# Kernel tuning notes

Measured on AMD Instinct MI355X. Metric: run time of the kernel, lower is better.

The kernel has to match this reference:

```python
import jax, jax.numpy as jnp
import numpy as np

N_NODES = 50000
IN_CH = 256
N_REL = 5
N_EDGES = 800000
LAST_SENSES = 25000
LAST_GLOBALS = 45000


def setup_inputs() -> dict:
    key = jax.random.key(0)
    ks = jax.random.split(key, 12)
    batch_x = jax.random.normal(ks[0], (N_NODES, IN_CH), dtype=jnp.float32)
    batch_edge_index = jax.random.randint(ks[1], (2, N_EDGES), 0, N_NODES)
    batch_edge_type = jax.random.randint(ks[2], (N_EDGES,), 0, N_REL)
    s = 1.0 / np.sqrt(IN_CH)
    comp = jax.random.normal(ks[3], (N_REL, N_REL), dtype=jnp.float32) * (1.0 / np.sqrt(N_REL))
    basis = jax.random.normal(ks[4], (N_REL, IN_CH, IN_CH), dtype=jnp.float32) * s
    root = jax.random.normal(ks[5], (IN_CH, IN_CH), dtype=jnp.float32) * s
    bias = jnp.zeros((IN_CH,), dtype=jnp.float32)
    n_glob = LAST_GLOBALS - LAST_SENSES
    Wg = jax.random.normal(ks[6], (n_glob, IN_CH), dtype=jnp.float32) * s
    bg = jnp.zeros((n_glob,), dtype=jnp.float32)
    Ws = jax.random.normal(ks[7], (LAST_SENSES, IN_CH), dtype=jnp.float32) * s
    bs = jnp.zeros((LAST_SENSES,), dtype=jnp.float32)
    return {
        'batch_x': batch_x,
        'batch_edge_index': batch_edge_index,
        'batch_edge_type': batch_edge_type,
        'comp': comp,
        'basis': basis,
        'root': root,
        'bias': bias,
        'Wg': Wg,
        'bg': bg,
        'Ws': Ws,
        'bs': bs,
    }


def _rgcn_conv(x, edge_index, edge_type, comp, basis, root, bias):
    # Basis decomposition: W_r = sum_b comp[r,b] * basis[b]  -> [R, d, d]
    R = comp.shape[0]
    N = x.shape[0]
    W = jnp.einsum('rb,bdf->rdf', comp, basis)
    # Transform all nodes by every relation weight once ([R,N,F]), then gather
    # per edge instead of doing an [E,d,d] weight gather.
    H = jnp.einsum('nd,rdf->rnf', x, W)
    src, dst = edge_index[0], edge_index[1]
    msgs = H[edge_type, src]                     # [E, F]
    seg = edge_type * N + dst                    # combined (relation, dst) id
    sums = jax.ops.segment_sum(msgs, seg, num_segments=R * N)
    cnt = jax.ops.segment_sum(jnp.ones((msgs.shape[0],), msgs.dtype), seg,
                              num_segments=R * N)
    mean = sums / jnp.maximum(cnt, 1.0)[:, None]  # per-relation mean aggregation
    agg = mean.reshape(R, N, -1).sum(axis=0)
    return agg + x @ root + bias


def reference(batch_x, batch_edge_index, batch_edge_type, comp, basis, root,
              bias, Wg, bg, Ws, bs):
    h = jax.nn.relu(_rgcn_conv(batch_x, batch_edge_index, batch_edge_type,
                               comp, basis, root, bias))
    x1 = h[0]                                    # current node embedding [F]
    logits_global = Wg @ x1 + bg
    logits_sense = Ws @ x1 + bs
    return (jax.nn.log_softmax(logits_global, axis=0),
            jax.nn.log_softmax(logits_sense, axis=0))
```

## Files before the change

kernel.cpp:

```cpp
#include <hip/hip_runtime.h>
#include <math.h>

#define N_NODES 50000
#define IN_CH 256
#define N_REL 5
#define N_EDGES 800000
#define N_GLOB 20000
#define N_SENSE 25000
#define N_OUT 45000
#define MAX_MATCH 256
#define NBLK_LOGITS (N_OUT / 4)
#define NBLK_GLOB (N_GLOB / 4)


__global__ void k_W(const float* __restrict__ comp,
                    const float* __restrict__ basis,
                    float* __restrict__ W,
                    float* __restrict__ sums,
                    int* __restrict__ ip) {
    int t = threadIdx.x, bid = blockIdx.x;
    if (bid == 0 && t < 8) ip[t] = 0;
    if (bid < 5) sums[bid * 256 + t] = 0.f;
    int idx = bid * 256 + t;
    int r = idx >> 16, df = idx & 65535;
    float acc = 0.f;
#pragma unroll
    for (int b = 0; b < N_REL; ++b)
        acc += comp[r * N_REL + b] * basis[b * (IN_CH * IN_CH) + df];
    W[idx] = acc;
}

__device__ __forceinline__ void record_edge(const int* ei, const int* et,
                                            int* ip, int e) {
    int t = et[e];
    int p = atomicAdd(&ip[0], 1);
    if (p < MAX_MATCH) {
        ip[8 + p] = ei[e];
        ip[8 + MAX_MATCH + p] = t;
    }
    atomicAdd(&ip[1 + t], 1);
}

__global__ void k_scan(const int* __restrict__ ei,
                       const int* __restrict__ et,
                       int* __restrict__ ip) {
    int e4 = blockIdx.x * 256 + threadIdx.x;
    if (e4 * 4 >= N_EDGES) return;
    int4 d = ((const int4*)(ei + N_EDGES))[e4];
    int e = e4 * 4;
    if (d.x == 0) record_edge(ei, et, ip, e);
    if (d.y == 0) record_edge(ei, et, ip, e + 1);
    if (d.z == 0) record_edge(ei, et, ip, e + 2);
    if (d.w == 0) record_edge(ei, et, ip, e + 3);
}

__global__ __launch_bounds__(1024) void k_msgs(const float* __restrict__ x,
                                               const float* __restrict__ W,
                                               const int* __restrict__ ip,
                                               float* __restrict__ sums) {
    int j = blockIdx.x;
    int m = ip[0]; if (m > MAX_MATCH) m = MAX_MATCH;
    if (j >= m) return;
    __shared__ float xrow[IN_CH];
    __shared__ float red[4][IN_CH];
    int tid = threadIdx.x;
    int f = tid & 255, c = tid >> 8;
    int s = ip[8 + j];
    int r = ip[8 + MAX_MATCH + j];
    if (c == 0) xrow[f] = x[(size_t)s * IN_CH + f];
    __syncthreads();
    const float* Wr = W + r * (IN_CH * IN_CH) + c * 64 * IN_CH;
    float acc = 0.f;
#pragma unroll 8
    for (int d = 0; d < 64; ++d) acc += xrow[c * 64 + d] * Wr[d * IN_CH + f];
    red[c][f] = acc;
    __syncthreads();
    if (c == 0)
        atomicAdd(&sums[r * IN_CH + f],
                  red[0][f] + red[1][f] + red[2][f] + red[3][f]);
}

__global__ __launch_bounds__(1024) void k_combine(const float* __restrict__ x,
                                                  const float* __restrict__ root,
                                                  const float* __restrict__ bias,
                                                  const float* __restrict__ sums,
                                                  const int* __restrict__ ip,
                                                  float* __restrict__ x1) {
    __shared__ float xrow[IN_CH];
    __shared__ float red[4][IN_CH];
    int tid = threadIdx.x;
    int f = tid & 255, c = tid >> 8;
    if (c == 0) xrow[f] = x[f];
    __syncthreads();
    const float* Rr = root + c * 64 * IN_CH;
    float acc = 0.f;
#pragma unroll 8
    for (int d = 0; d < 64; ++d) acc += xrow[c * 64 + d] * Rr[d * IN_CH + f];
    red[c][f] = acc;
    __syncthreads();
    if (c == 0) {
        float a = bias[f] + red[0][f] + red[1][f] + red[2][f] + red[3][f];
#pragma unroll
        for (int r = 0; r < N_REL; ++r)
            a += sums[r * IN_CH + f] / fmaxf((float)ip[1 + r], 1.0f);
        x1[f] = fmaxf(a, 0.f);
    }
}

__global__ void k_logits(const float* __restrict__ Wg,
                         const float* __restrict__ bg,
                         const float* __restrict__ Ws,
                         const float* __restrict__ bs,
                         const float* __restrict__ x1,
                         float* __restrict__ out,
                         float* __restrict__ pmax,
                         float* __restrict__ psum) {
    __shared__ float sx[IN_CH];
    __shared__ float sl[4];
    int tid = threadIdx.x;
    sx[tid] = x1[tid];
    __syncthreads();
    int lane = tid & 63, w = tid >> 6;
    int row = blockIdx.x * 4 + w;
    const float4* wr;
    float b;
    if (row < N_GLOB) {
        wr = (const float4*)(Wg + (size_t)row * IN_CH);
        b = bg[row];
    } else {
        int r2 = row - N_GLOB;
        wr = (const float4*)(Ws + (size_t)r2 * IN_CH);
        b = bs[r2];
    }
    float4 wv = wr[lane];
    float4 xv = ((const float4*)sx)[lane];
    float s = wv.x * xv.x + wv.y * xv.y + wv.z * xv.z + wv.w * xv.w;
#pragma unroll
    for (int off = 32; off > 0; off >>= 1) s += __shfl_down(s, off);
    if (lane == 0) { float l = s + b; out[row] = l; sl[w] = l; }
    __syncthreads();
    if (tid == 0) {
        float m4 = fmaxf(fmaxf(sl[0], sl[1]), fmaxf(sl[2], sl[3]));
        float s4 = expf(sl[0] - m4) + expf(sl[1] - m4) +
                   expf(sl[2] - m4) + expf(sl[3] - m4);
        pmax[blockIdx.x] = m4;
        psum[blockIdx.x] = s4;
    }
}

__global__ void k_stats(const float* __restrict__ pmax,
                        const float* __restrict__ psum,
                        float* __restrict__ stats) {
    __shared__ float rm[256], rs[256];
    int seg = blockIdx.x;
    int off = seg ? NBLK_GLOB : 0;
    int n = seg ? (NBLK_LOGITS - NBLK_GLOB) : NBLK_GLOB;
    int tid = threadIdx.x;
    float m = -3.4e38f, s = 0.f;
    for (int i = tid; i < n; i += 256) {
        float mi = pmax[off + i], si = psum[off + i];
        float M = fmaxf(m, mi);
        s = s * expf(m - M) + si * expf(mi - M);
        m = M;
    }
    rm[tid] = m; rs[tid] = s; __syncthreads();
    for (int h = 128; h > 0; h >>= 1) {
        if (tid < h) {
            float m2 = rm[tid + h], s2 = rs[tid + h];
            float M = fmaxf(rm[tid], m2);
            rs[tid] = rs[tid] * expf(rm[tid] - M) + s2 * expf(m2 - M);
            rm[tid] = M;
        }
        __syncthreads();
    }
    if (tid == 0) { stats[seg * 2] = rm[0]; stats[seg * 2 + 1] = logf(rs[0]); }
}

__global__ void k_final(float* __restrict__ out, const float* __restrict__ stats) {
    int i = blockIdx.x * 256 + threadIdx.x;
    if (i >= N_OUT) return;
    int seg = (i >= N_GLOB) ? 1 : 0;
    out[i] = out[i] - stats[seg * 2] - stats[seg * 2 + 1];
}

extern "C" void kernel_launch(void* const* d_in, const int* in_sizes, int n_in,
                              void* d_out, int out_size, void* d_ws, size_t ws_size,
                              hipStream_t stream) {
    const float* x     = (const float*)d_in[0];
    const int*   ei    = (const int*)  d_in[1];
    const int*   et    = (const int*)  d_in[2];
    const float* comp  = (const float*)d_in[3];
    const float* basis = (const float*)d_in[4];
    const float* root  = (const float*)d_in[5];
    const float* bias  = (const float*)d_in[6];
    const float* Wg    = (const float*)d_in[7];
    const float* bg    = (const float*)d_in[8];
    const float* Wsn   = (const float*)d_in[9];
    const float* bs    = (const float*)d_in[10];
    float* out = (float*)d_out;

    float* base  = (float*)d_ws;
    float* W     = base;
    float* sums  = base + 327680;
    float* x1    = base + 328960;
    float* stats = base + 329216;
    int*   ip    = (int*)(base + 329220);
    float* pmax  = base + 330240;
    float* psum  = base + 341490;

    k_W      <<<(N_REL * IN_CH * IN_CH) / 256, 256, 0, stream>>>(comp, basis, W, sums, ip);
    k_scan   <<<(N_EDGES / 4 + 255) / 256, 256, 0, stream>>>(ei, et, ip);
    k_msgs   <<<MAX_MATCH, 1024, 0, stream>>>(x, W, ip, sums);
    k_combine<<<1, 1024, 0, stream>>>(x, root, bias, sums, ip, x1);
    k_logits <<<NBLK_LOGITS, 256, 0, stream>>>(Wg, bg, Wsn, bs, x1, out, pmax, psum);
    k_stats  <<<2, 256, 0, stream>>>(pmax, psum, stats);
    k_final  <<<(N_OUT + 255) / 256, 256, 0, stream>>>(out, stats);
}
```

Baseline: 158.4 us.

## Fuse pipeline into four kernels with last-block reductions and persistent logits grid

Merges the W construction, edge scan and root matvec into one launch, folds the combine step into the message kernel via a last-block-done counter, and fuses logits with the softmax statistics reduction in a grid-strided kernel that processes four rows per wave. The aim is to remove launch overhead and idle single-block kernels from a latency-bound chain of seven launches. It adds atomics, a memset, and threadfence-based completion detection, which bring ordering and correctness risks.

```diff
diff --git a/kernel.cpp b/kernel.cpp
--- a/kernel.cpp
+++ b/kernel.cpp
@@ -5,33 +5,38 @@
 #define IN_CH 256
 #define N_REL 5
 #define N_EDGES 800000
+#define N_E4 200000
 #define N_GLOB 20000
 #define N_SENSE 25000
 #define N_OUT 45000
 #define MAX_MATCH 256
-#define NBLK_LOGITS (N_OUT / 4)
-#define NBLK_GLOB (N_GLOB / 4)
-
-
-__global__ void k_W(const float* __restrict__ comp,
-                    const float* __restrict__ basis,
-                    float* __restrict__ W,
-                    float* __restrict__ sums,
-                    int* __restrict__ ip) {
-    int t = threadIdx.x, bid = blockIdx.x;
-    if (bid == 0 && t < 8) ip[t] = 0;
-    if (bid < 5) sums[bid * 256 + t] = 0.f;
-    int idx = bid * 256 + t;
-    int r = idx >> 16, df = idx & 65535;
-    float acc = 0.f;
-#pragma unroll
-    for (int b = 0; b < N_REL; ++b)
-        acc += comp[r * N_REL + b] * basis[b * (IN_CH * IN_CH) + df];
-    W[idx] = acc;
-}
-
-__device__ __forceinline__ void record_edge(const int* ei, const int* et,
-                                            int* ip, int e) {
+#define N_QUAD 11250
+#define Q_GLOB 5000
+
+#define G2 1024
+#define G3 2048
+
+#define WS_SUMS 327680
+#define WS_ROOTACC 328960
+#define WS_IP 329216
+#define WS_X1 329760
+#define WS_STATS 330016
+#define WS_PM 330048
+
+__device__ __forceinline__ float aload(const float* p) {
+    return __hip_atomic_load(p, __ATOMIC_RELAXED, __HIP_MEMORY_SCOPE_AGENT);
+}
+
+__device__ __forceinline__ void omerge(float& m, float& s, float m2, float s2) {
+    float M = fmaxf(m, m2);
+    if (M == -INFINITY) return;
+    s = s * expf(m - M) + s2 * expf(m2 - M);
+    m = M;
+}
+
+__device__ __forceinline__ void rec(const int* __restrict__ ei,
+                                    const int* __restrict__ et,
+                                    int* __restrict__ ip, int e) {
     int t = et[e];
     int p = atomicAdd(&ip[0], 1);
     if (p < MAX_MATCH) {
@@ -41,146 +46,177 @@
     atomicAdd(&ip[1 + t], 1);
 }
 
-__global__ void k_scan(const int* __restrict__ ei,
-                       const int* __restrict__ et,
-                       int* __restrict__ ip) {
-    int e4 = blockIdx.x * 256 + threadIdx.x;
-    if (e4 * 4 >= N_EDGES) return;
-    int4 d = ((const int4*)(ei + N_EDGES))[e4];
-    int e = e4 * 4;
-    if (d.x == 0) record_edge(ei, et, ip, e);
-    if (d.y == 0) record_edge(ei, et, ip, e + 1);
-    if (d.z == 0) record_edge(ei, et, ip, e + 2);
-    if (d.w == 0) record_edge(ei, et, ip, e + 3);
-}
-
-__global__ __launch_bounds__(1024) void k_msgs(const float* __restrict__ x,
-                                               const float* __restrict__ W,
-                                               const int* __restrict__ ip,
-                                               float* __restrict__ sums) {
-    int j = blockIdx.x;
+__global__ __launch_bounds__(256) void k1(const float* __restrict__ x,
+                                          const int* __restrict__ ei,
+                                          const int* __restrict__ et,
+                                          const float* __restrict__ comp,
+                                          const float* __restrict__ basis,
+                                          const float* __restrict__ root,
+                                          float* __restrict__ base) {
+    float* W = base;
+    float* rootacc = base + WS_ROOTACC;
+    int* ip = (int*)(base + WS_IP);
+    int bid = blockIdx.x, tid = threadIdx.x;
+    if (bid < 1280) {
+        int idx = bid * 256 + tid;
+        int r = idx >> 16, df = idx & 65535;
+        float acc = 0.f;
+#pragma unroll
+        for (int b = 0; b < N_REL; ++b)
+            acc += comp[r * N_REL + b] * basis[b * (IN_CH * IN_CH) + df];
+        W[idx] = acc;
+    } else if (bid < 2062) {
+        int e4 = (bid - 1280) * 256 + tid;
+        if (e4 < N_E4) {
+            int4 d = ((const int4*)(ei + N_EDGES))[e4];
+            int e = e4 * 4;
+            if (d.x == 0) rec(ei, et, ip, e);
+            if (d.y == 0) rec(ei, et, ip, e + 1);
+            if (d.z == 0) rec(ei, et, ip, e + 2);
+            if (d.w == 0) rec(ei, et, ip, e + 3);
+        }
+    } else {
+        int c = bid - 2062;
+        const float* xp = x + c * 64;
+        const float* rp = root + c * 64 * IN_CH + tid;
+        float acc = 0.f;
+#pragma unroll 8
+        for (int d = 0; d < 64; ++d) acc += xp[d] * rp[d * IN_CH];
+        atomicAdd(&rootacc[tid], acc);
+    }
+}
+
+__global__ __launch_bounds__(256) void k2(const float* __restrict__ x,
+                                          const float* __restrict__ bias,
+                                          float* __restrict__ base) {
+    float* W = base;
+    float* sums = base + WS_SUMS;
+    float* rootacc = base + WS_ROOTACC;
+    int* ip = (int*)(base + WS_IP);
+    float* x1 = base + WS_X1;
+    int tid = threadIdx.x, bid = blockIdx.x;
+
     int m = ip[0]; if (m > MAX_MATCH) m = MAX_MATCH;
-    if (j >= m) return;
-    __shared__ float xrow[IN_CH];
-    __shared__ float red[4][IN_CH];
-    int tid = threadIdx.x;
-    int f = tid & 255, c = tid >> 8;
-    int s = ip[8 + j];
-    int r = ip[8 + MAX_MATCH + j];
-    if (c == 0) xrow[f] = x[(size_t)s * IN_CH + f];
-    __syncthreads();
-    const float* Wr = W + r * (IN_CH * IN_CH) + c * 64 * IN_CH;
-    float acc = 0.f;
+    if (bid < 4 * m) {
+        int j = bid >> 2, c = bid & 3;
+        int s = ip[8 + j];
+        int r = ip[8 + MAX_MATCH + j];
+        const float* xp = x + (size_t)s * IN_CH + c * 64;
+        const float* wp = W + r * (IN_CH * IN_CH) + c * 64 * IN_CH + tid;
+        float acc = 0.f;
 #pragma unroll 8
-    for (int d = 0; d < 64; ++d) acc += xrow[c * 64 + d] * Wr[d * IN_CH + f];
-    red[c][f] = acc;
-    __syncthreads();
-    if (c == 0)
-        atomicAdd(&sums[r * IN_CH + f],
-                  red[0][f] + red[1][f] + red[2][f] + red[3][f]);
-}
-
-__global__ __launch_bounds__(1024) void k_combine(const float* __restrict__ x,
-                                                  const float* __restrict__ root,
-                                                  const float* __restrict__ bias,
-                                                  const float* __restrict__ sums,
-                                                  const int* __restrict__ ip,
-                                                  float* __restrict__ x1) {
-    __shared__ float xrow[IN_CH];
-    __shared__ float red[4][IN_CH];
-    int tid = threadIdx.x;
-    int f = tid & 255, c = tid >> 8;
-    if (c == 0) xrow[f] = x[f];
-    __syncthreads();
-    const float* Rr = root + c * 64 * IN_CH;
-    float acc = 0.f;
-#pragma unroll 8
-    for (int d = 0; d < 64; ++d) acc += xrow[c * 64 + d] * Rr[d * IN_CH + f];
-    red[c][f] = acc;
-    __syncthreads();
-    if (c == 0) {
-        float a = bias[f] + red[0][f] + red[1][f] + red[2][f] + red[3][f];
-#pragma unroll
-        for (int r = 0; r < N_REL; ++r)
-            a += sums[r * IN_CH + f] / fmaxf((float)ip[1 + r], 1.0f);
-        x1[f] = fmaxf(a, 0.f);
-    }
-}
-
-__global__ void k_logits(const float* __restrict__ Wg,
-                         const float* __restrict__ bg,
-                         const float* __restrict__ Ws,
-                         const float* __restrict__ bs,
-                         const float* __restrict__ x1,
-                         float* __restrict__ out,
-                         float* __restrict__ pmax,
-                         float* __restrict__ psum) {
-    __shared__ float sx[IN_CH];
-    __shared__ float sl[4];
-    int tid = threadIdx.x;
+        for (int d = 0; d < 64; ++d) acc += xp[d] * wp[d * IN_CH];
+        atomicAdd(&sums[r * IN_CH + tid], acc);
+    }
+    __shared__ int slast;
+    __syncthreads();
+    if (tid == 0) {
+        __threadfence();
+        int prev = atomicAdd(&ip[6], 1);
+        slast = (prev == G2 - 1) ? 1 : 0;
+    }
+    __syncthreads();
+    if (!slast) return;
+    __threadfence();
+    float a = bias[tid] + rootacc[tid];
+#pragma unroll
+    for (int r = 0; r < N_REL; ++r)
+        a += aload(&sums[r * IN_CH + tid]) / fmaxf((float)ip[1 + r], 1.f);
+    x1[tid] = fmaxf(a, 0.f);
+}
+
+__global__ __launch_bounds__(256) void k3(const float* __restrict__ Wg,
+                                          const float* __restrict__ bg,
+                                          const float* __restrict__ Ws,
+                                          const float* __restrict__ bs,
+                                          float* __restrict__ out,
+                                          float* __restrict__ base) {
+    __shared__ __align__(16) float sx[IN_CH];
+    __shared__ float rbuf[4][4];
+    __shared__ int slast;
+    __shared__ float rm[256], rs[256];
+    float* x1 = base + WS_X1;
+    int* ip = (int*)(base + WS_IP);
+    float* stats = base + WS_STATS;
+    float* pm_g = base + WS_PM;
+    float* ps_g = pm_g + G3;
+    float* pm_s = ps_g + G3;
+    float* ps_s = pm_s + G3;
+
+    int tid = threadIdx.x, bid = blockIdx.x;
     sx[tid] = x1[tid];
     __syncthreads();
-    int lane = tid & 63, w = tid >> 6;
-    int row = blockIdx.x * 4 + w;
-    const float4* wr;
-    float b;
-    if (row < N_GLOB) {
-        wr = (const float4*)(Wg + (size_t)row * IN_CH);
-        b = bg[row];
-    } else {
-        int r2 = row - N_GLOB;
-        wr = (const float4*)(Ws + (size_t)r2 * IN_CH);
-        b = bs[r2];
-    }
-    float4 wv = wr[lane];
+
+    const int lane = tid & 63, w = tid >> 6;
     float4 xv = ((const float4*)sx)[lane];
-    float s = wv.x * xv.x + wv.y * xv.y + wv.z * xv.z + wv.w * xv.w;
-#pragma unroll
-    for (int off = 32; off > 0; off >>= 1) s += __shfl_down(s, off);
-    if (lane == 0) { float l = s + b; out[row] = l; sl[w] = l; }
+    float mg = -INFINITY, sg = 0.f, ms = -INFINITY, ss = 0.f;
+
+    for (int q = bid * 4 + w; q < N_QUAD; q += G3 * 4) {
+        const float* mat; const float* bv; int rl;
+        if (q < Q_GLOB) { mat = Wg; bv = bg; rl = q * 4; }
+        else            { mat = Ws; bv = bs; rl = q * 4 - N_GLOB; }
+        const float4* p = (const float4*)(mat + (size_t)rl * IN_CH);
+        float4 a0 = p[lane], a1 = p[64 + lane], a2 = p[128 + lane], a3 = p[192 + lane];
+        float d0 = a0.x * xv.x + a0.y * xv.y + a0.z * xv.z + a0.w * xv.w;
+        float d1 = a1.x * xv.x + a1.y * xv.y + a1.z * xv.z + a1.w * xv.w;
+        float d2 = a2.x * xv.x + a2.y * xv.y + a2.z * xv.z + a2.w * xv.w;
+        float d3 = a3.x * xv.x + a3.y * xv.y + a3.z * xv.z + a3.w * xv.w;
+#pragma unroll
+        for (int off = 32; off; off >>= 1) {
+            d0 += __shfl_xor(d0, off); d1 += __shfl_xor(d1, off);
+            d2 += __shfl_xor(d2, off); d3 += __shfl_xor(d3, off);
+        }
+        float4 bq = *(const float4*)(bv + rl);
+        float l0 = d0 + bq.x, l1 = d1 + bq.y, l2 = d2 + bq.z, l3 = d3 + bq.w;
+        if (lane == 0) ((float4*)out)[q] = make_float4(l0, l1, l2, l3);
+        float lm = fmaxf(fmaxf(l0, l1), fmaxf(l2, l3));
+        float le = expf(l0 - lm) + expf(l1 - lm) + expf(l2 - lm) + expf(l3 - lm);
+        if (q < Q_GLOB) omerge(mg, sg, lm, le);
+        else            omerge(ms, ss, lm, le);
+    }
+    if (lane == 0) { rbuf[w][0] = mg; rbuf[w][1] = sg; rbuf[w][2] = ms; rbuf[w][3] = ss; }
     __syncthreads();
     if (tid == 0) {
-        float m4 = fmaxf(fmaxf(sl[0], sl[1]), fmaxf(sl[2], sl[3]));
-        float s4 = expf(sl[0] - m4) + expf(sl[1] - m4) +
-                   expf(sl[2] - m4) + expf(sl[3] - m4);
-        pmax[blockIdx.x] = m4;
-        psum[blockIdx.x] = s4;
-    }
-}
-
-__global__ void k_stats(const float* __restrict__ pmax,
-                        const float* __restrict__ psum,
-                        float* __restrict__ stats) {
-    __shared__ float rm[256], rs[256];
-    int seg = blockIdx.x;
-    int off = seg ? NBLK_GLOB : 0;
-    int n = seg ? (NBLK_LOGITS - NBLK_GLOB) : NBLK_GLOB;
-    int tid = threadIdx.x;
-    float m = -3.4e38f, s = 0.f;
-    for (int i = tid; i < n; i += 256) {
-        float mi = pmax[off + i], si = psum[off + i];
-        float M = fmaxf(m, mi);
-        s = s * expf(m - M) + si * expf(mi - M);
-        m = M;
-    }
-    rm[tid] = m; rs[tid] = s; __syncthreads();
-    for (int h = 128; h > 0; h >>= 1) {
-        if (tid < h) {
-            float m2 = rm[tid + h], s2 = rs[tid + h];
-            float M = fmaxf(rm[tid], m2);
-            rs[tid] = rs[tid] * expf(rm[tid] - M) + s2 * expf(m2 - M);
-            rm[tid] = M;
+        float M0 = rbuf[0][0], S0 = rbuf[0][1], M1 = rbuf[0][2], S1 = rbuf[0][3];
+#pragma unroll
+        for (int i = 1; i < 4; ++i) {
+            omerge(M0, S0, rbuf[i][0], rbuf[i][1]);
+            omerge(M1, S1, rbuf[i][2], rbuf[i][3]);
         }
+        pm_g[bid] = M0; ps_g[bid] = S0; pm_s[bid] = M1; ps_s[bid] = S1;
+        __threadfence();
+        int prev = atomicAdd(&ip[7], 1);
+        slast = (prev == G3 - 1) ? 1 : 0;
+    }
+    __syncthreads();
+    if (!slast) return;
+    __threadfence();
+
+    float M = -INFINITY, S = 0.f;
+    for (int i = tid; i < G3; i += 256) omerge(M, S, aload(&pm_g[i]), aload(&ps_g[i]));
+    rm[tid] = M; rs[tid] = S; __syncthreads();
+    for (int h = 128; h; h >>= 1) {
+        if (tid < h) omerge(rm[tid], rs[tid], rm[tid + h], rs[tid + h]);
         __syncthreads();
     }
-    if (tid == 0) { stats[seg * 2] = rm[0]; stats[seg * 2 + 1] = logf(rs[0]); }
-}
-
-__global__ void k_final(float* __restrict__ out, const float* __restrict__ stats) {
+    if (tid == 0) stats[0] = rm[0] + logf(rs[0]);
+    __syncthreads();
+    M = -INFINITY; S = 0.f;
+    for (int i = tid; i < G3; i += 256) omerge(M, S, aload(&pm_s[i]), aload(&ps_s[i]));
+    rm[tid] = M; rs[tid] = S; __syncthreads();
+    for (int h = 128; h; h >>= 1) {
+        if (tid < h) omerge(rm[tid], rs[tid], rm[tid + h], rs[tid + h]);
+        __syncthreads();
+    }
+    if (tid == 0) stats[1] = rm[0] + logf(rs[0]);
+}
+
+__global__ __launch_bounds__(256) void k4(float* __restrict__ out,
+                                          const float* __restrict__ base) {
+    const float* stats = base + WS_STATS;
     int i = blockIdx.x * 256 + threadIdx.x;
     if (i >= N_OUT) return;
-    int seg = (i >= N_GLOB) ? 1 : 0;
-    out[i] = out[i] - stats[seg * 2] - stats[seg * 2 + 1];
+    out[i] -= (i < N_GLOB) ? stats[0] : stats[1];
 }
 
 extern "C" void kernel_launch(void* const* d_in, const int* in_sizes, int n_in,
@@ -197,22 +233,13 @@
     const float* bg    = (const float*)d_in[8];
     const float* Wsn   = (const float*)d_in[9];
     const float* bs    = (const float*)d_in[10];
-    float* out = (float*)d_out;
-
-    float* base  = (float*)d_ws;
-    float* W     = base;
-    float* sums  = base + 327680;
-    float* x1    = base + 328960;
-    float* stats = base + 329216;
-    int*   ip    = (int*)(base + 329220);
-    float* pmax  = base + 330240;
-    float* psum  = base + 341490;
-
-    k_W      <<<(N_REL * IN_CH * IN_CH) / 256, 256, 0, stream>>>(comp, basis, W, sums, ip);
-    k_scan   <<<(N_EDGES / 4 + 255) / 256, 256, 0, stream>>>(ei, et, ip);
-    k_msgs   <<<MAX_MATCH, 1024, 0, stream>>>(x, W, ip, sums);
-    k_combine<<<1, 1024, 0, stream>>>(x, root, bias, sums, ip, x1);
-    k_logits <<<NBLK_LOGITS, 256, 0, stream>>>(Wg, bg, Wsn, bs, x1, out, pmax, psum);
-    k_stats  <<<2, 256, 0, stream>>>(pmax, psum, stats);
-    k_final  <<<(N_OUT + 255) / 256, 256, 0, stream>>>(out, stats);
-}
+    float* out  = (float*)d_out;
+    float* base = (float*)d_ws;
+
+    hipMemsetAsync(base + WS_SUMS, 0, 6176, stream);
+
+    k1<<<2066, 256, 0, stream>>>(x, ei, et, comp, basis, root, base);
+    k2<<<G2,   256, 0, stream>>>(x, bias, base);
+    k3<<<G3,   256, 0, stream>>>(Wg, bg, Wsn, bs, out, base);
+    k4<<<(N_OUT + 255) / 256, 256, 0, stream>>>(out, base);
+}
```

Result: slower. 218.5 us (+37.9%).
